# Kernel tuning notes

Hardware: AMD Instinct MI355X
Metric: run time of the kernel (lower is better)

The kernel has to match this reference:

```python
import jax, jax.numpy as jnp
import numpy as np
from jax import lax

T, B, I, H = 1024, 512, 128, 256


def setup_inputs() -> dict:
    key = jax.random.key(0)
    ks = jax.random.split(key, 7)
    s = 1.0 / np.sqrt(H)
    inputs = jax.random.normal(ks[0], (T, B, I), dtype=jnp.float32)
    # PyTorch LSTM params, gate order (i, f, g, o)
    W_ih = jax.random.uniform(ks[1], (4 * H, I), minval=-s, maxval=s, dtype=jnp.float32)
    W_hh = jax.random.uniform(ks[2], (4 * H, H), minval=-s, maxval=s, dtype=jnp.float32)
    b_ih = jax.random.uniform(ks[3], (4 * H,), minval=-s, maxval=s, dtype=jnp.float32)
    b_hh = jax.random.uniform(ks[4], (4 * H,), minval=-s, maxval=s, dtype=jnp.float32)
    W_out = jax.random.uniform(ks[5], (1, H), minval=-s, maxval=s, dtype=jnp.float32)
    b_out = jax.random.uniform(ks[6], (1,), minval=-s, maxval=s, dtype=jnp.float32)
    return {"inputs": inputs, "W_ih": W_ih, "W_hh": W_hh, "b_ih": b_ih,
            "b_hh": b_hh, "W_out": W_out, "b_out": b_out}


def reference(inputs, W_ih, W_hh, b_ih, b_hh, W_out, b_out):
    # inputs: (T, B, I). mask from last feature channel, as in the torch code.
    mask = (inputs[..., -1] > 0).astype(inputs.dtype)  # (T, B)
    # Precompute input projections for all timesteps (hoisted out of recurrence).
    x_proj = jnp.einsum('tbi,gi->tbg', inputs, W_ih) + b_ih + b_hh  # (T, B, 4H)
    h0 = jnp.zeros((inputs.shape[1], H), inputs.dtype)
    c0 = h0

    def step(carry, xs):
        h, c = carry
        xp, m = xs
        gates = xp + h @ W_hh.T  # (B, 4H)
        i, f, g, o = jnp.split(gates, 4, axis=-1)
        i = jax.nn.sigmoid(i)
        f = jax.nn.sigmoid(f)
        g = jnp.tanh(g)
        o = jax.nn.sigmoid(o)
        c_new = f * c + i * g
        h_new = o * jnp.tanh(c_new)
        m = m[:, None]
        # state is masked AFTER the cell; lstm_out keeps the unmasked h
        return (m * h_new, m * c_new), h_new

    _, hs = lax.scan(step, (h0, c0), (x_proj, mask))
    last_h = hs[-1]  # unmasked output of final step (lstm_out[-1])
    likelihood = last_h @ W_out.T + b_out  # (B, 1)
    return likelihood.sum(-1)  # (B,)
```

## Files before the change

kernel.cpp:

```cpp
#include <hip/hip_runtime.h>
#include <hip/hip_fp16.h>
#include <math.h>

#define T_ 1024
#define B_ 512
#define I_ 128
#define H_ 256
#define K_ 384
#define KP_ 192

typedef _Float16 h2_t __attribute__((ext_vector_type(2)));

__device__ __forceinline__ float fsigmoid(float x) {
  return 1.0f / (1.0f + __expf(-x));
}
__device__ __forceinline__ float ftanh(float x) {
  float ax = fabsf(x);
  float e = __expf(-2.0f * ax);
  float t = (1.0f - e) / (1.0f + e);
  return copysignf(t, x);
}
__device__ __forceinline__ void dot2(float& acc, unsigned int w, unsigned int v) {
  acc = __builtin_amdgcn_fdot2(__builtin_bit_cast(h2_t, w),
                               __builtin_bit_cast(h2_t, v), acc, false);
}

__global__ void prep_kernel(const float* __restrict__ W_ih,
                            const float* __restrict__ W_hh,
                            const float* __restrict__ b_ih,
                            const float* __restrict__ b_hh,
                            __half* __restrict__ Whq,
                            float4* __restrict__ biasq,
                            int* __restrict__ sstart) {
  const int j = (int)threadIdx.x;
  const int kp = (int)blockIdx.x;
  const int k0 = 2 * kp, k1 = 2 * kp + 1;
  __half* dst = Whq + ((size_t)(kp * H_ + j)) * 8;
#pragma unroll
  for (int g = 0; g < 4; ++g) {
    const int row = g * H_ + j;
    float w0, w1;
    if (k0 < I_) {
      w0 = W_ih[row * I_ + k0];
      w1 = W_ih[row * I_ + k1];
    } else {
      w0 = W_hh[row * H_ + (k0 - I_)];
      w1 = W_hh[row * H_ + (k1 - I_)];
    }
    dst[g * 2 + 0] = __float2half(w0);
    dst[g * 2 + 1] = __float2half(w1);
  }
  if (kp == 0) {
    biasq[j] = make_float4(b_ih[j] + b_hh[j],
                           b_ih[H_ + j] + b_hh[H_ + j],
                           b_ih[2 * H_ + j] + b_hh[2 * H_ + j],
                           b_ih[3 * H_ + j] + b_hh[3 * H_ + j]);
    sstart[j] = 0;
    sstart[H_ + j] = 0;
  }
}

__global__ __launch_bounds__(1024) void scan_kernel(
    const float* __restrict__ x,
    int* __restrict__ sstart) {
  const int tid = (int)threadIdx.x;
  const int b = tid & (B_ - 1);
  const int half = tid >> 9;
  const int t0 = (int)blockIdx.x * 8 + half * 4;
  int best = 0;
#pragma unroll
  for (int it = 0; it < 4; ++it) {
    const int t = t0 + it;
    if (t <= T_ - 2) {
      const float xv = x[((long)t * B_ + b) * I_ + (I_ - 1)];
      if (xv <= 0.0f) best = t + 1;
    }
  }
  if (best > 0) atomicMax(sstart + b, best);
}

__global__ __launch_bounds__(1024) void lstm_kernel(
    const float* __restrict__ x,
    const uint4* __restrict__ W4,
    const float4* __restrict__ biasq,
    const int* __restrict__ sstart,
    const float* __restrict__ W_out,
    const float* __restrict__ b_out,
    float* __restrict__ out) {
  __shared__ __align__(16) __half v[2][K_];
  __shared__ __align__(16) float4 part[4][2][H_];
  __shared__ float msk[2];
  __shared__ float red[8];
  const int tid = (int)threadIdx.x;
  const int kq = tid >> 8;
  const int j = tid & (H_ - 1);
  const int b0 = (int)blockIdx.x * 2;

  const float4 bias = biasq[j];
  const int ts = min(sstart[b0], sstart[b0 + 1]);

  if (kq < 2) v[kq][I_ + j] = __float2half(0.0f);
  if (tid < 2 * I_) {
    const int sb = tid >> 7, ii = tid & (I_ - 1);
    const float xv = x[((long)ts * B_ + (b0 + sb)) * I_ + ii];
    v[sb][ii] = __float2half(xv);
    if (ii == I_ - 1) msk[sb] = (xv > 0.0f) ? 1.0f : 0.0f;
  }

  float c = 0.0f, lasth = 0.0f;
  const uint4* __restrict__ wbase = W4 + (size_t)(kq * (KP_ / 4)) * H_ + j;
  const uint4* __restrict__ v0q = (const uint4*)(&v[0][kq * (K_ / 4)]);
  const uint4* __restrict__ v1q = (const uint4*)(&v[1][kq * (K_ / 4)]);

  for (int t = ts; t < T_; ++t) {
    __syncthreads();
    float m = 0.0f;
    if (kq < 2) m = msk[kq];

    float4 acc0 = make_float4(0.f, 0.f, 0.f, 0.f);
    float4 acc1 = make_float4(0.f, 0.f, 0.f, 0.f);
    const uint4* wp = wbase;
#pragma unroll 4
    for (int i = 0; i < 12; ++i) {
      const uint4 va = v0q[i];
      const uint4 vb = v1q[i];
      const uint4 w0 = wp[0];
      const uint4 w1 = wp[H_];
      const uint4 w2 = wp[2 * H_];
      const uint4 w3 = wp[3 * H_];
      wp += 4 * H_;
      dot2(acc0.x, w0.x, va.x); dot2(acc0.y, w0.y, va.x);
      dot2(acc0.z, w0.z, va.x); dot2(acc0.w, w0.w, va.x);
      dot2(acc1.x, w0.x, vb.x); dot2(acc1.y, w0.y, vb.x);
      dot2(acc1.z, w0.z, vb.x); dot2(acc1.w, w0.w, vb.x);
      dot2(acc0.x, w1.x, va.y); dot2(acc0.y, w1.y, va.y);
      dot2(acc0.z, w1.z, va.y); dot2(acc0.w, w1.w, va.y);
      dot2(acc1.x, w1.x, vb.y); dot2(acc1.y, w1.y, vb.y);
      dot2(acc1.z, w1.z, vb.y); dot2(acc1.w, w1.w, vb.y);
      dot2(acc0.x, w2.x, va.z); dot2(acc0.y, w2.y, va.z);
      dot2(acc0.z, w2.z, va.z); dot2(acc0.w, w2.w, va.z);
      dot2(acc1.x, w2.x, vb.z); dot2(acc1.y, w2.y, vb.z);
      dot2(acc1.z, w2.z, vb.z); dot2(acc1.w, w2.w, vb.z);
      dot2(acc0.x, w3.x, va.w); dot2(acc0.y, w3.y, va.w);
      dot2(acc0.z, w3.z, va.w); dot2(acc0.w, w3.w, va.w);
      dot2(acc1.x, w3.x, vb.w); dot2(acc1.y, w3.y, vb.w);
      dot2(acc1.z, w3.z, vb.w); dot2(acc1.w, w3.w, vb.w);
    }
    part[kq][0][j] = acc0;
    part[kq][1][j] = acc1;
    __syncthreads();

    if (kq < 2) {
      const float4 p0 = part[0][kq][j];
      const float4 p1 = part[1][kq][j];
      const float4 p2 = part[2][kq][j];
      const float4 p3 = part[3][kq][j];
      const float gi = fsigmoid(p0.x + p1.x + p2.x + p3.x + bias.x);
      const float gf = fsigmoid(p0.y + p1.y + p2.y + p3.y + bias.y);
      const float gg = ftanh(p0.z + p1.z + p2.z + p3.z + bias.z);
      const float go = fsigmoid(p0.w + p1.w + p2.w + p3.w + bias.w);
      const float cn = gf * c + gi * gg;
      const float hn = go * ftanh(cn);
      if (t == T_ - 1) lasth = hn;
      c = m * cn;
      v[kq][I_ + j] = __float2half(m * hn);
    }
    if (t + 1 < T_ && tid < 2 * I_) {
      const int sb = tid >> 7, ii = tid & (I_ - 1);
      const float xv = x[((long)(t + 1) * B_ + (b0 + sb)) * I_ + ii];
      v[sb][ii] = __float2half(xv);
      if (ii == I_ - 1) msk[sb] = (xv > 0.0f) ? 1.0f : 0.0f;
    }
  }

  float p = (kq < 2) ? W_out[j] * lasth : 0.0f;
#pragma unroll
  for (int off = 32; off > 0; off >>= 1) p += __shfl_down(p, off, 64);
  const int wave = tid >> 6;
  if (wave < 8 && (tid & 63) == 0) red[wave] = p;
  __syncthreads();
  if (tid == 0)   out[b0]     = red[0] + red[1] + red[2] + red[3] + b_out[0];
  if (tid == 256) out[b0 + 1] = red[4] + red[5] + red[6] + red[7] + b_out[0];
}

extern "C" void kernel_launch(void* const* d_in, const int* in_sizes, int n_in,
                              void* d_out, int out_size, void* d_ws, size_t ws_size,
                              hipStream_t stream) {
  (void)in_sizes; (void)n_in; (void)out_size; (void)ws_size;
  const float* x     = (const float*)d_in[0];
  const float* W_ih  = (const float*)d_in[1];
  const float* W_hh  = (const float*)d_in[2];
  const float* b_ih  = (const float*)d_in[3];
  const float* b_hh  = (const float*)d_in[4];
  const float* W_out = (const float*)d_in[5];
  const float* b_out = (const float*)d_in[6];
  float* out = (float*)d_out;

  char* ws = (char*)d_ws;
  __half* Whq   = (__half*)ws;
  float4* biasq = (float4*)(ws + (size_t)KP_ * H_ * 8 * sizeof(__half));
  int*    sst   = (int*)((char*)biasq + (size_t)H_ * sizeof(float4));

  hipLaunchKernelGGL(prep_kernel, dim3(KP_), dim3(H_), 0, stream,
                     W_ih, W_hh, b_ih, b_hh, Whq, biasq, sst);
  hipLaunchKernelGGL(scan_kernel, dim3(T_ / 8), dim3(1024), 0, stream,
                     x, sst);
  hipLaunchKernelGGL(lstm_kernel, dim3(B_ / 2), dim3(1024), 0, stream,
                     x, (const uint4*)Whq, biasq, sst, W_out, b_out, out);
}
```

Before: 392.0 us.

## Fuse prep and mask scan; cache recurrent weights in registers and LDS

Merges weight conversion and the last-reset-timestep scan into one launch. Each window block writes a per-batch partial maximum, which the LSTM kernel reduces with wave shuffles, so the atomics and the separate zeroing of the start array go away. The LSTM kernel now keeps the first 8 weight vectors per thread in registers and the next 7 in LDS, cutting global weight reads in every step. It also skips the hidden-state product on the first step, where h is zero. The catch is a heavier prologue per block and much more LDS use, which limits residency to one block per CU.

```diff
diff --git a/kernel.cpp b/kernel.cpp
--- a/kernel.cpp
+++ b/kernel.cpp
@@ -8,6 +8,9 @@
 #define H_ 256
 #define K_ 384
 #define KP_ 192
+#define REG_N 8
+#define LDS_N 7
+#define NWIN 64
 
 typedef _Float16 h2_t __attribute__((ext_vector_type(2)));
 
@@ -25,81 +28,113 @@
                                __builtin_bit_cast(h2_t, v), acc, false);
 }
 
-__global__ void prep_kernel(const float* __restrict__ W_ih,
-                            const float* __restrict__ W_hh,
-                            const float* __restrict__ b_ih,
-                            const float* __restrict__ b_hh,
-                            __half* __restrict__ Whq,
-                            float4* __restrict__ biasq,
-                            int* __restrict__ sstart) {
-  const int j = (int)threadIdx.x;
-  const int kp = (int)blockIdx.x;
-  const int k0 = 2 * kp, k1 = 2 * kp + 1;
-  __half* dst = Whq + ((size_t)(kp * H_ + j)) * 8;
-#pragma unroll
-  for (int g = 0; g < 4; ++g) {
-    const int row = g * H_ + j;
-    float w0, w1;
-    if (k0 < I_) {
-      w0 = W_ih[row * I_ + k0];
-      w1 = W_ih[row * I_ + k1];
-    } else {
-      w0 = W_hh[row * H_ + (k0 - I_)];
-      w1 = W_hh[row * H_ + (k1 - I_)];
-    }
-    dst[g * 2 + 0] = __float2half(w0);
-    dst[g * 2 + 1] = __float2half(w1);
-  }
-  if (kp == 0) {
-    biasq[j] = make_float4(b_ih[j] + b_hh[j],
-                           b_ih[H_ + j] + b_hh[H_ + j],
-                           b_ih[2 * H_ + j] + b_hh[2 * H_ + j],
-                           b_ih[3 * H_ + j] + b_hh[3 * H_ + j]);
-    sstart[j] = 0;
-    sstart[H_ + j] = 0;
-  }
-}
-
-__global__ __launch_bounds__(1024) void scan_kernel(
+#define ACC8(W, VA, VB, C)                                      \
+  dot2(acc0.x, (W).x, (VA).C); dot2(acc0.y, (W).y, (VA).C);     \
+  dot2(acc0.z, (W).z, (VA).C); dot2(acc0.w, (W).w, (VA).C);     \
+  dot2(acc1.x, (W).x, (VB).C); dot2(acc1.y, (W).y, (VB).C);     \
+  dot2(acc1.z, (W).z, (VB).C); dot2(acc1.w, (W).w, (VB).C);
+
+__global__ __launch_bounds__(1024) void prep_scan_kernel(
+    const float* __restrict__ W_ih,
+    const float* __restrict__ W_hh,
+    const float* __restrict__ b_ih,
+    const float* __restrict__ b_hh,
     const float* __restrict__ x,
-    int* __restrict__ sstart) {
+    __half* __restrict__ Whq,
+    float4* __restrict__ biasq,
+    int* __restrict__ partial) {
+  __shared__ int smax[2][B_];
   const int tid = (int)threadIdx.x;
-  const int b = tid & (B_ - 1);
-  const int half = tid >> 9;
-  const int t0 = (int)blockIdx.x * 8 + half * 4;
-  int best = 0;
-#pragma unroll
-  for (int it = 0; it < 4; ++it) {
-    const int t = t0 + it;
-    if (t <= T_ - 2) {
-      const float xv = x[((long)t * B_ + b) * I_ + (I_ - 1)];
-      if (xv <= 0.0f) best = t + 1;
-    }
-  }
-  if (best > 0) atomicMax(sstart + b, best);
+  const int bx = (int)blockIdx.x;
+
+  if (bx < 48) {
+    const int kp = bx * 4 + (tid >> 8);
+    const int j = tid & (H_ - 1);
+    const int k0 = 2 * kp, k1 = 2 * kp + 1;
+    __half* dst = Whq + ((size_t)(kp * H_ + j)) * 8;
+#pragma unroll
+    for (int g = 0; g < 4; ++g) {
+      const int row = g * H_ + j;
+      float w0, w1;
+      if (k0 < I_) {
+        w0 = W_ih[row * I_ + k0];
+        w1 = W_ih[row * I_ + k1];
+      } else {
+        w0 = W_hh[row * H_ + (k0 - I_)];
+        w1 = W_hh[row * H_ + (k1 - I_)];
+      }
+      dst[g * 2 + 0] = __float2half(w0);
+      dst[g * 2 + 1] = __float2half(w1);
+    }
+    if (bx == 0 && tid < H_) {
+      const int jj = tid;
+      biasq[jj] = make_float4(b_ih[jj] + b_hh[jj],
+                              b_ih[H_ + jj] + b_hh[H_ + jj],
+                              b_ih[2 * H_ + jj] + b_hh[2 * H_ + jj],
+                              b_ih[3 * H_ + jj] + b_hh[3 * H_ + jj]);
+    }
+  } else {
+    const int win = bx - 48;
+    const int b = tid & (B_ - 1);
+    const int half = tid >> 9;
+    int best = 0;
+    const float* __restrict__ px = x + (long)b * I_ + (I_ - 1);
+#pragma unroll
+    for (int it = 0; it < 8; ++it) {
+      const int t = win * 16 + half * 8 + it;
+      if (t <= T_ - 2) {
+        const float xv = px[(long)t * ((long)B_ * I_)];
+        if (xv <= 0.0f) best = t + 1;
+      }
+    }
+    smax[half][b] = best;
+    __syncthreads();
+    if (tid < B_) partial[win * B_ + tid] = max(smax[0][tid], smax[1][tid]);
+  }
 }
 
 __global__ __launch_bounds__(1024) void lstm_kernel(
     const float* __restrict__ x,
     const uint4* __restrict__ W4,
     const float4* __restrict__ biasq,
-    const int* __restrict__ sstart,
+    const int* __restrict__ partial,
     const float* __restrict__ W_out,
     const float* __restrict__ b_out,
     float* __restrict__ out) {
   __shared__ __align__(16) __half v[2][K_];
   __shared__ __align__(16) float4 part[4][2][H_];
+  __shared__ __align__(16) uint4 lw[LDS_N][1024];
   __shared__ float msk[2];
   __shared__ float red[8];
+  __shared__ int sh_ts;
   const int tid = (int)threadIdx.x;
   const int kq = tid >> 8;
   const int j = tid & (H_ - 1);
   const int b0 = (int)blockIdx.x * 2;
 
   const float4 bias = biasq[j];
-  const int ts = min(sstart[b0], sstart[b0 + 1]);
-
+  const uint4* __restrict__ wbase = W4 + (size_t)(kq * (KP_ / 4)) * H_ + j;
+
+  uint4 rw[REG_N];
+#pragma unroll
+  for (int n = 0; n < REG_N; ++n) rw[n] = wbase[(size_t)n * H_];
+#pragma unroll
+  for (int m = 0; m < LDS_N; ++m) lw[m][tid] = wbase[(size_t)(REG_N + m) * H_];
+
+  if (tid < 64) {
+    const int2 pv = *(const int2*)(partial + tid * B_ + b0);
+    int s0 = pv.x, s1 = pv.y;
+#pragma unroll
+    for (int off = 32; off > 0; off >>= 1) {
+      s0 = max(s0, __shfl_down(s0, off, 64));
+      s1 = max(s1, __shfl_down(s1, off, 64));
+    }
+    if (tid == 0) sh_ts = min(s0, s1);
+  }
   if (kq < 2) v[kq][I_ + j] = __float2half(0.0f);
+  __syncthreads();
+  const int ts = sh_ts;
+
   if (tid < 2 * I_) {
     const int sb = tid >> 7, ii = tid & (I_ - 1);
     const float xv = x[((long)ts * B_ + (b0 + sb)) * I_ + ii];
@@ -108,7 +143,6 @@
   }
 
   float c = 0.0f, lasth = 0.0f;
-  const uint4* __restrict__ wbase = W4 + (size_t)(kq * (KP_ / 4)) * H_ + j;
   const uint4* __restrict__ v0q = (const uint4*)(&v[0][kq * (K_ / 4)]);
   const uint4* __restrict__ v1q = (const uint4*)(&v[1][kq * (K_ / 4)]);
 
@@ -116,35 +150,51 @@
     __syncthreads();
     float m = 0.0f;
     if (kq < 2) m = msk[kq];
+    const int nskip = (t != ts) ? 48 : ((kq == 0) ? 48 : (kq == 1) ? 16 : 0);
 
     float4 acc0 = make_float4(0.f, 0.f, 0.f, 0.f);
     float4 acc1 = make_float4(0.f, 0.f, 0.f, 0.f);
-    const uint4* wp = wbase;
-#pragma unroll 4
-    for (int i = 0; i < 12; ++i) {
-      const uint4 va = v0q[i];
-      const uint4 vb = v1q[i];
-      const uint4 w0 = wp[0];
-      const uint4 w1 = wp[H_];
-      const uint4 w2 = wp[2 * H_];
-      const uint4 w3 = wp[3 * H_];
-      wp += 4 * H_;
-      dot2(acc0.x, w0.x, va.x); dot2(acc0.y, w0.y, va.x);
-      dot2(acc0.z, w0.z, va.x); dot2(acc0.w, w0.w, va.x);
-      dot2(acc1.x, w0.x, vb.x); dot2(acc1.y, w0.y, vb.x);
-      dot2(acc1.z, w0.z, vb.x); dot2(acc1.w, w0.w, vb.x);
-      dot2(acc0.x, w1.x, va.y); dot2(acc0.y, w1.y, va.y);
-      dot2(acc0.z, w1.z, va.y); dot2(acc0.w, w1.w, va.y);
-      dot2(acc1.x, w1.x, vb.y); dot2(acc1.y, w1.y, vb.y);
-      dot2(acc1.z, w1.z, vb.y); dot2(acc1.w, w1.w, vb.y);
-      dot2(acc0.x, w2.x, va.z); dot2(acc0.y, w2.y, va.z);
-      dot2(acc0.z, w2.z, va.z); dot2(acc0.w, w2.w, va.z);
-      dot2(acc1.x, w2.x, vb.z); dot2(acc1.y, w2.y, vb.z);
-      dot2(acc1.z, w2.z, vb.z); dot2(acc1.w, w2.w, vb.z);
-      dot2(acc0.x, w3.x, va.w); dot2(acc0.y, w3.y, va.w);
-      dot2(acc0.z, w3.z, va.w); dot2(acc0.w, w3.w, va.w);
-      dot2(acc1.x, w3.x, vb.w); dot2(acc1.y, w3.y, vb.w);
-      dot2(acc1.z, w3.z, vb.w); dot2(acc1.w, w3.w, vb.w);
+    {
+      const uint4 va = v0q[0], vb = v1q[0];
+      ACC8(rw[0], va, vb, x); ACC8(rw[1], va, vb, y);
+      ACC8(rw[2], va, vb, z); ACC8(rw[3], va, vb, w);
+    }
+    {
+      const uint4 va = v0q[1], vb = v1q[1];
+      ACC8(rw[4], va, vb, x); ACC8(rw[5], va, vb, y);
+      ACC8(rw[6], va, vb, z); ACC8(rw[7], va, vb, w);
+    }
+    {
+      const uint4 va = v0q[2], vb = v1q[2];
+      const uint4 w0 = lw[0][tid], w1 = lw[1][tid];
+      const uint4 w2 = lw[2][tid], w3 = lw[3][tid];
+      ACC8(w0, va, vb, x); ACC8(w1, va, vb, y);
+      ACC8(w2, va, vb, z); ACC8(w3, va, vb, w);
+    }
+    {
+      const uint4 va = v0q[3], vb = v1q[3];
+      const uint4 w0 = lw[4][tid], w1 = lw[5][tid], w2 = lw[6][tid];
+      ACC8(w0, va, vb, x); ACC8(w1, va, vb, y); ACC8(w2, va, vb, z);
+    }
+    if (nskip == 48) {
+      {
+        const uint4 va = v0q[3], vb = v1q[3];
+        const uint4 w3 = wbase[(size_t)15 * H_];
+        ACC8(w3, va, vb, w);
+      }
+#pragma unroll 2
+      for (int i = 4; i < 12; ++i) {
+        const uint4 va = v0q[i], vb = v1q[i];
+        const uint4* wp = wbase + (size_t)(4 * i) * H_;
+        { const uint4 w = wp[0];      ACC8(w, va, vb, x); }
+        { const uint4 w = wp[H_];     ACC8(w, va, vb, y); }
+        { const uint4 w = wp[2 * H_]; ACC8(w, va, vb, z); }
+        { const uint4 w = wp[3 * H_]; ACC8(w, va, vb, w); }
+      }
+    } else if (nskip == 16) {
+      const uint4 va = v0q[3], vb = v1q[3];
+      const uint4 w3 = wbase[(size_t)15 * H_];
+      ACC8(w3, va, vb, w);
     }
     part[kq][0][j] = acc0;
     part[kq][1][j] = acc1;
@@ -199,12 +249,10 @@
   char* ws = (char*)d_ws;
   __half* Whq   = (__half*)ws;
   float4* biasq = (float4*)(ws + (size_t)KP_ * H_ * 8 * sizeof(__half));
-  int*    sst   = (int*)((char*)biasq + (size_t)H_ * sizeof(float4));
-
-  hipLaunchKernelGGL(prep_kernel, dim3(KP_), dim3(H_), 0, stream,
-                     W_ih, W_hh, b_ih, b_hh, Whq, biasq, sst);
-  hipLaunchKernelGGL(scan_kernel, dim3(T_ / 8), dim3(1024), 0, stream,
-                     x, sst);
+  int*    prt   = (int*)((char*)biasq + (size_t)H_ * sizeof(float4));
+
+  hipLaunchKernelGGL(prep_scan_kernel, dim3(48 + NWIN), dim3(1024), 0, stream,
+                     W_ih, W_hh, b_ih, b_hh, x, Whq, biasq, prt);
   hipLaunchKernelGGL(lstm_kernel, dim3(B_ / 2), dim3(1024), 0, stream,
-                     x, (const uint4*)Whq, biasq, sst, W_out, b_out, out);
-}
+                     x, (const uint4*)Whq, biasq, prt, W_out, b_out, out);
+}
```

Result: no change. 387.7 us (-1.1%).
